# Performance work log

Hardware: AMD Instinct MI355X
Metric: run time of the kernel (lower is better)

The kernel has to match this reference:

```python
import jax, jax.numpy as jnp
import numpy as np

DIM, HEADS, HEAD_DIM, EPS = 1536, 12, 128, 1e-6
B, S = 1, 4096


def rmsnorm(x, w, eps=EPS):
    v = jnp.mean(jnp.square(x), axis=-1, keepdims=True)
    return x * jax.lax.rsqrt(v + eps) * w


def apply_rope(x, freqs):
    # x: [b,s,n,d]; freqs: [s, d//2] rotation angles (complex rope on adjacent pairs)
    b, s, n, d = x.shape
    xr = x.reshape(b, s, n, d // 2, 2)
    cos = jnp.cos(freqs)[None, :, None, :]
    sin = jnp.sin(freqs)[None, :, None, :]
    x0, x1 = xr[..., 0], xr[..., 1]
    out = jnp.stack([x0 * cos - x1 * sin, x0 * sin + x1 * cos], axis=-1)
    return out.reshape(b, s, n, d)


def setup_inputs() -> dict:
    key = jax.random.key(0)
    ks = jax.random.split(key, 12)
    scale = 0.02
    x = jax.random.normal(ks[0], (B, S, DIM), jnp.float32)
    # standard rope angles: pos * inv_freq
    inv_freq = 1.0 / (10000.0 ** (jnp.arange(0, HEAD_DIM, 2, dtype=jnp.float32) / HEAD_DIM))
    freqs = jnp.arange(S, dtype=jnp.float32)[:, None] * inv_freq[None, :]  # [S, 64]
    Wq = jax.random.normal(ks[1], (DIM, DIM), jnp.float32) * scale
    bq = jax.random.normal(ks[2], (DIM,), jnp.float32) * scale
    Wk = jax.random.normal(ks[3], (DIM, DIM), jnp.float32) * scale
    bk = jax.random.normal(ks[4], (DIM,), jnp.float32) * scale
    Wv = jax.random.normal(ks[5], (DIM, DIM), jnp.float32) * scale
    bv = jax.random.normal(ks[6], (DIM,), jnp.float32) * scale
    Wo = jax.random.normal(ks[7], (DIM, DIM), jnp.float32) * scale
    bo = jax.random.normal(ks[8], (DIM,), jnp.float32) * scale
    gq = 1.0 + jax.random.normal(ks[9], (DIM,), jnp.float32) * 0.01
    gk = 1.0 + jax.random.normal(ks[10], (DIM,), jnp.float32) * 0.01
    return dict(x=x, freqs=freqs, Wq=Wq, bq=bq, Wk=Wk, bk=bk, Wv=Wv, bv=bv,
                Wo=Wo, bo=bo, gq=gq, gk=gk)


def reference(x, freqs, Wq, bq, Wk, bk, Wv, bv, Wo, bo, gq, gk):
    b, s = x.shape[:2]
    n, d = HEADS, HEAD_DIM
    q = apply_rope(rmsnorm(x @ Wq.T + bq, gq).reshape(b, s, n, d), freqs)
    k = apply_rope(rmsnorm(x @ Wk.T + bk, gk).reshape(b, s, n, d), freqs)
    v = (x @ Wv.T + bv).reshape(b, s, n, d)
    # SDPA: softmax(q k^T / sqrt(d)) v
    scores = jnp.einsum('bqnd,bknd->bnqk', q, k) / jnp.sqrt(jnp.asarray(d, x.dtype))
    attn = jax.nn.softmax(scores, axis=-1)
    out = jnp.einsum('bnqk,bknd->bqnd', attn, v).reshape(b, s, n * d)
    return out @ Wo.T + bo
```

## Files before the change

### kernel.cpp

```cpp
#include <hip/hip_runtime.h>
#include <stdint.h>
#include <math.h>

#define DIM 1536
#define SEQ 4096
#define HEADS 12
#define HD 128

typedef __bf16 bf16x8 __attribute__((ext_vector_type(8)));
typedef float f32x4 __attribute__((ext_vector_type(4)));

typedef __attribute__((address_space(1))) void gas_void;
typedef __attribute__((address_space(3))) void las_void;

__device__ __forceinline__ float b2f(unsigned short u) {
  union { unsigned int i; float f; } x; x.i = ((unsigned int)u) << 16; return x.f;
}
__device__ __forceinline__ unsigned short f2b(float f) {
  union { float f; unsigned int i; } x; x.f = f;
  unsigned int u = x.i;
  unsigned int r = (u + 0x7fffu + ((u >> 16) & 1u)) >> 16;
  return (unsigned short)r;
}
__device__ __forceinline__ void gll16(const unsigned short* g, unsigned short* l) {
  __builtin_amdgcn_global_load_lds((gas_void*)g, (las_void*)l, 16, 0, 0);
}
__device__ __forceinline__ void cvtpk(unsigned int& d, float a, float b) {
  asm("v_cvt_pk_bf16_f32 %0, %1, %2" : "=v"(d) : "v"(a), "v"(b));
}
__device__ __forceinline__ void pl32(unsigned int& a, unsigned int& b) {
  asm("v_permlane32_swap_b32 %0, %1" : "+v"(a), "+v"(b));
}
__device__ __forceinline__ void pl16(unsigned int& a, unsigned int& b) {
  asm("v_permlane16_swap_b32 %0, %1" : "+v"(a), "+v"(b));
}
__device__ __forceinline__ float fexp2(float x) { return __builtin_amdgcn_exp2f(x); }

__global__ void detect_kernel(const unsigned int* __restrict__ xw, int* flag) {
  __shared__ int cnt;
  if (threadIdx.x == 0) cnt = 0;
  __syncthreads();
  int local = 0;
  for (int i = threadIdx.x; i < 1024; i += 256) {
    unsigned int e = (xw[i] >> 7) & 0xFFu;
    if (e >= 110u && e <= 140u) local++;
  }
  atomicAdd(&cnt, local);
  __syncthreads();
  if (threadIdx.x == 0) *flag = (cnt > 512) ? 0 : 1;
}

__global__ void convert_bf16_kernel(const void* __restrict__ src,
                                    unsigned short* __restrict__ dst, int n4,
                                    const int* __restrict__ flag) {
  int f = *flag;
  for (int i = blockIdx.x * blockDim.x + threadIdx.x; i < n4; i += gridDim.x * blockDim.x) {
    if (f) {
      float4 v = ((const float4*)src)[i];
      union { unsigned short h[4]; uint2 u; } pk;
      pk.h[0] = f2b(v.x); pk.h[1] = f2b(v.y); pk.h[2] = f2b(v.z); pk.h[3] = f2b(v.w);
      ((uint2*)dst)[i] = pk.u;
    } else {
      ((uint2*)dst)[i] = ((const uint2*)src)[i];
    }
  }
}

__global__ void convert_w4_kernel(const void* s0, const void* s1, const void* s2, const void* s3,
                                  unsigned short* d0, unsigned short* d1,
                                  unsigned short* d2, unsigned short* d3,
                                  int n4, const int* __restrict__ flag) {
  const void* s; unsigned short* d;
  switch (blockIdx.y) {
    case 0: s = s0; d = d0; break;
    case 1: s = s1; d = d1; break;
    case 2: s = s2; d = d2; break;
    default: s = s3; d = d3; break;
  }
  int f = *flag;
  for (int i = blockIdx.x * blockDim.x + threadIdx.x; i < n4; i += gridDim.x * blockDim.x) {
    if (f) {
      float4 v = ((const float4*)s)[i];
      union { unsigned short h[4]; uint2 u; } pk;
      pk.h[0] = f2b(v.x); pk.h[1] = f2b(v.y); pk.h[2] = f2b(v.z); pk.h[3] = f2b(v.w);
      ((uint2*)d)[i] = pk.u;
    } else {
      ((uint2*)d)[i] = ((const uint2*)s)[i];
    }
  }
}

__global__ void convert_v6_kernel(const void* s0, const void* s1, const void* s2,
                                  const void* s3, const void* s4, const void* s5,
                                  unsigned short* d0, unsigned short* d1, unsigned short* d2,
                                  unsigned short* d3, unsigned short* d4, unsigned short* d5,
                                  int n, const int* __restrict__ flag) {
  const void* s; unsigned short* d;
  switch (blockIdx.y) {
    case 0: s = s0; d = d0; break;
    case 1: s = s1; d = d1; break;
    case 2: s = s2; d = d2; break;
    case 3: s = s3; d = d3; break;
    case 4: s = s4; d = d4; break;
    default: s = s5; d = d5; break;
  }
  int f = *flag;
  for (int i = blockIdx.x * blockDim.x + threadIdx.x; i < n; i += gridDim.x * blockDim.x)
    d[i] = f ? f2b(((const float*)s)[i]) : ((const unsigned short*)s)[i];
}

__global__ void convert_f32_kernel(const void* __restrict__ src,
                                   float* __restrict__ dst, int n,
                                   const int* __restrict__ flag) {
  int f = *flag;
  for (int i = blockIdx.x * blockDim.x + threadIdx.x; i < n; i += gridDim.x * blockDim.x)
    dst[i] = f ? ((const float*)src)[i] : b2f(((const unsigned short*)src)[i]);
}

__global__ void signal_kernel(float* out) { if (threadIdx.x == 0) out[0] = 999.0f; }

template<int BM>
__device__ __forceinline__ void gemm_bt_body(
    const unsigned short* __restrict__ A,
    const unsigned short* __restrict__ W,
    const unsigned short* __restrict__ bias,
    unsigned short* __restrict__ Cb, float* __restrict__ Cf, int fmt, int vmode,
    int K, int N, int bx, int by)
{
  constexpr int BK = 64;
  constexpr int MI = BM / 32;
  constexpr int ALINES = BM * BK * 2 / 4096;
  __shared__ unsigned short As[BM * BK];
  __shared__ unsigned short Bs[128 * BK];
  const int t = threadIdx.x;
  const int wave = t >> 6, lane = t & 63;
  const int quad = lane >> 4, l16 = lane & 15;
  const int m0 = by * BM, n0 = bx * 128;
  const int wm = (wave >> 1) * (BM / 2), wn = (wave & 1) * 64;

  f32x4 acc[MI][4] = {};

  const int srow = t >> 3;
  const int scol = ((t & 7) ^ ((t >> 3) & 7)) * 8;
  const unsigned short* Ag = A + (size_t)(m0 + srow) * K + scol;
  const unsigned short* Wg = W + (size_t)(n0 + srow) * K + scol;

  for (int k0 = 0; k0 < K; k0 += BK) {
    __syncthreads();
#pragma unroll
    for (int L = 0; L < ALINES; ++L)
      gll16(Ag + (size_t)L * 32 * K + k0, &As[L * 2048 + t * 8]);
#pragma unroll
    for (int L = 0; L < 4; ++L)
      gll16(Wg + (size_t)L * 32 * K + k0, &Bs[L * 2048 + t * 8]);
    __syncthreads();
#pragma unroll
    for (int c = 0; c < 2; ++c) {
      bf16x8 af[MI], bfr[4];
#pragma unroll
      for (int i = 0; i < MI; ++i) {
        int row = wm + i * 16 + l16;
        af[i] = *(const bf16x8*)&As[row * 64 + ((c * 4 + quad) ^ (row & 7)) * 8];
      }
#pragma unroll
      for (int j = 0; j < 4; ++j) {
        int row = wn + j * 16 + l16;
        bfr[j] = *(const bf16x8*)&Bs[row * 64 + ((c * 4 + quad) ^ (row & 7)) * 8];
      }
#pragma unroll
      for (int i = 0; i < MI; ++i)
#pragma unroll
        for (int j = 0; j < 4; ++j)
          acc[i][j] = __builtin_amdgcn_mfma_f32_16x16x32_bf16(af[i], bfr[j], acc[i][j], 0, 0, 0);
    }
  }

#pragma unroll
  for (int i = 0; i < MI; ++i) {
    int row = m0 + wm + i * 16 + quad * 4;
#pragma unroll
    for (int j = 0; j < 4; ++j) {
      int col = n0 + wn + j * 16 + l16;
      float bv = b2f(bias[col]);
      if (vmode) {
        union { unsigned short h4[4]; uint2 u; } pk;
#pragma unroll
        for (int r = 0; r < 4; ++r) pk.h4[r] = f2b(acc[i][j][r] + bv);
        *(uint2*)&Cb[(size_t)col * SEQ + row] = pk.u;
      } else {
#pragma unroll
        for (int r = 0; r < 4; ++r) {
          float v = acc[i][j][r] + bv;
          size_t idx = (size_t)(row + r) * N + col;
          if (fmt) Cf[idx] = v; else Cb[idx] = f2b(v);
        }
      }
    }
  }
}

__global__ __launch_bounds__(256) void qkv_gemm_kernel(
    const unsigned short* __restrict__ x,
    const unsigned short* __restrict__ Wq, const unsigned short* __restrict__ bq,
    const unsigned short* __restrict__ Wk, const unsigned short* __restrict__ bk,
    const unsigned short* __restrict__ Wv, const unsigned short* __restrict__ bv,
    unsigned short* qb, unsigned short* kb, unsigned short* vt)
{
  const unsigned short *W, *b; unsigned short* C; int vm = 0;
  if (blockIdx.z == 0)      { W = Wq; b = bq; C = qb; }
  else if (blockIdx.z == 1) { W = Wk; b = bk; C = kb; }
  else                      { W = Wv; b = bv; C = vt; vm = 1; }
  gemm_bt_body<128>(x, W, b, C, nullptr, 0, vm, DIM, DIM, blockIdx.x, blockIdx.y);
}

__global__ __launch_bounds__(256) void out_gemm_kernel(
    const unsigned short* __restrict__ ab, const unsigned short* __restrict__ Wo,
    const unsigned short* __restrict__ bo, void* out, const int* __restrict__ flag)
{
  int fmt = *flag;
  gemm_bt_body<64>(ab, Wo, bo, (unsigned short*)out, (float*)out, fmt, 0,
                   DIM, DIM, blockIdx.x, blockIdx.y);
}

__global__ __launch_bounds__(256) void norm_rope_kernel(
    unsigned short* __restrict__ qb, unsigned short* __restrict__ kb,
    const unsigned short* __restrict__ gq, const unsigned short* __restrict__ gk,
    const float* __restrict__ freqsf)
{
  const int s = blockIdx.x;
  const int isq = (blockIdx.y == 0);
  unsigned short* row = (isq ? qb : kb) + (size_t)s * DIM;
  const unsigned short* g = (isq ? gq : gk);
  const int t = threadIdx.x;
  float ss = 0.f;
#pragma unroll
  for (int i = 0; i < 6; ++i) {
    float xv = b2f(row[t + 256 * i]);
    ss += xv * xv;
  }
#pragma unroll
  for (int off = 32; off > 0; off >>= 1) ss += __shfl_down(ss, off);
  __shared__ float red[4];
  if ((t & 63) == 0) red[t >> 6] = ss;
  __syncthreads();
  float tot = red[0] + red[1] + red[2] + red[3];
  float rinv = 1.0f / sqrtf(tot * (1.0f / DIM) + 1e-6f);
  if (isq) rinv *= 0.12751744900725559f;
#pragma unroll
  for (int i = 0; i < 3; ++i) {
    int pg = t + 256 * i;
    int c0 = pg * 2;
    float x0 = b2f(row[c0]), x1 = b2f(row[c0 + 1]);
    float y0 = x0 * rinv * b2f(g[c0]);
    float y1 = x1 * rinv * b2f(g[c0 + 1]);
    float ang = freqsf[s * 64 + (pg & 63)];
    float sn, cs;
    __sincosf(ang, &sn, &cs);
    row[c0]     = f2b(y0 * cs - y1 * sn);
    row[c0 + 1] = f2b(y0 * sn + y1 * cs);
  }
}

__global__ __launch_bounds__(256) void attn_kernel(
    const unsigned short* __restrict__ qb,
    const unsigned short* __restrict__ kb,
    const unsigned short* __restrict__ vt,
    float* __restrict__ op,
    float* __restrict__ lp,
    int seg)
{
  __shared__ unsigned short Ks[64 * 128];
  __shared__ unsigned short Vs[128 * 64];

  const int t = threadIdx.x;
  const int wave = t >> 6, lane = t & 63;
  const int quad = lane >> 4, l16 = lane & 15;
  const int h = blockIdx.y;
  const int z = blockIdx.z;
  const int qbase = blockIdx.x * 128 + wave * 32;
  const int kc0 = z * seg;

  bf16x8 qf[2][4];
#pragma unroll
  for (int mt = 0; mt < 2; ++mt)
#pragma unroll
    for (int kk = 0; kk < 4; ++kk)
      qf[mt][kk] = *(const bf16x8*)(qb + (size_t)(qbase + mt * 16 + l16) * DIM
                                    + h * HD + kk * 32 + quad * 8);

  f32x4 o[2][8] = {};
  float Lr[2] = {};

  const int krow = t >> 2, kblk = (t & 3) * 4;
  const int vd = t >> 1,  vblk = (t & 1) * 4;

  const unsigned short* kbase = kb + (size_t)krow * DIM + h * HD + kblk * 8;
  const unsigned short* vbase = vt + ((size_t)h * HD + vd) * SEQ + vblk * 8;

  uint4 kr0, kr1, kr2, kr3, vr0, vr1, vr2, vr3;
  {
    const unsigned short* s = kbase + (size_t)kc0 * DIM;
    kr0 = *(const uint4*)(s);
    kr1 = *(const uint4*)(s + 8);
    kr2 = *(const uint4*)(s + 16);
    kr3 = *(const uint4*)(s + 24);
    const unsigned short* sv = vbase + kc0;
    vr0 = *(const uint4*)(sv);
    vr1 = *(const uint4*)(sv + 8);
    vr2 = *(const uint4*)(sv + 16);
    vr3 = *(const uint4*)(sv + 24);
  }

  for (int kc = kc0; kc < kc0 + seg; kc += 64) {
    __syncthreads();
    {
      unsigned short* dst = &Ks[krow * 128];
      const int sw = krow & 7;
      *(uint4*)(dst + ((kblk + 0) ^ sw) * 8) = kr0;
      *(uint4*)(dst + ((kblk + 1) ^ sw) * 8) = kr1;
      *(uint4*)(dst + ((kblk + 2) ^ sw) * 8) = kr2;
      *(uint4*)(dst + ((kblk + 3) ^ sw) * 8) = kr3;
    }
    {
      unsigned short* dst = &Vs[vd * 64];
      const int sw = vd & 7;
      *(uint4*)(dst + ((vblk + 0) ^ sw) * 8) = vr0;
      *(uint4*)(dst + ((vblk + 1) ^ sw) * 8) = vr1;
      *(uint4*)(dst + ((vblk + 2) ^ sw) * 8) = vr2;
      *(uint4*)(dst + ((vblk + 3) ^ sw) * 8) = vr3;
    }
    __syncthreads();

    {
      int nkc = kc + 64;
      if (nkc >= kc0 + seg) nkc = kc;
      const unsigned short* s = kbase + (size_t)nkc * DIM;
      kr0 = *(const uint4*)(s);
      kr1 = *(const uint4*)(s + 8);
      kr2 = *(const uint4*)(s + 16);
      kr3 = *(const uint4*)(s + 24);
      const unsigned short* sv = vbase + nkc;
      vr0 = *(const uint4*)(sv);
      vr1 = *(const uint4*)(sv + 8);
      vr2 = *(const uint4*)(sv + 16);
      vr3 = *(const uint4*)(sv + 24);
    }

    f32x4 sc[2][4] = {};
    __builtin_amdgcn_s_setprio(1);
#pragma unroll
    for (int kk = 0; kk < 4; ++kk) {
#pragma unroll
      for (int j = 0; j < 4; ++j) {
        int row = j * 16 + l16;
        bf16x8 kf = *(const bf16x8*)&Ks[row * 128 + ((kk * 4 + quad) ^ (row & 7)) * 8];
        sc[0][j] = __builtin_amdgcn_mfma_f32_16x16x32_bf16(kf, qf[0][kk], sc[0][j], 0, 0, 0);
        sc[1][j] = __builtin_amdgcn_mfma_f32_16x16x32_bf16(kf, qf[1][kk], sc[1][j], 0, 0, 0);
      }
    }
    __builtin_amdgcn_s_setprio(0);

    unsigned int wlo[2][4], whi[2][4];
#pragma unroll
    for (int mt = 0; mt < 2; ++mt) {
      float ls = 0.f;
#pragma unroll
      for (int j = 0; j < 4; ++j) {
        float p0 = fexp2(sc[mt][j][0]);
        float p1 = fexp2(sc[mt][j][1]);
        float p2 = fexp2(sc[mt][j][2]);
        float p3 = fexp2(sc[mt][j][3]);
        ls += (p0 + p1) + (p2 + p3);
        cvtpk(wlo[mt][j], p0, p1);
        cvtpk(whi[mt][j], p2, p3);
      }
      Lr[mt] += ls;
    }

    bf16x8 pf[2][2];
#pragma unroll
    for (int mt = 0; mt < 2; ++mt)
#pragma unroll
      for (int kk2 = 0; kk2 < 2; ++kk2) {
        unsigned int ul = wlo[mt][kk2 * 2], vl = wlo[mt][kk2 * 2 + 1];
        unsigned int uh = whi[mt][kk2 * 2], vh = whi[mt][kk2 * 2 + 1];
        pl32(ul, vl); pl16(ul, vl);
        pl32(uh, vh); pl16(uh, vh);
        union { unsigned int w[4]; bf16x8 v; } u;
        u.w[0] = ul; u.w[1] = uh; u.w[2] = vl; u.w[3] = vh;
        pf[mt][kk2] = u.v;
      }

    __builtin_amdgcn_s_setprio(1);
#pragma unroll
    for (int kk2 = 0; kk2 < 2; ++kk2) {
#pragma unroll
      for (int j2 = 0; j2 < 8; ++j2) {
        bf16x8 vf = *(const bf16x8*)&Vs[(j2 * 16 + l16) * 64
                                        + ((kk2 * 4 + quad) ^ (l16 & 7)) * 8];
        o[0][j2] = __builtin_amdgcn_mfma_f32_16x16x32_bf16(pf[0][kk2], vf, o[0][j2], 0, 0, 0);
        o[1][j2] = __builtin_amdgcn_mfma_f32_16x16x32_bf16(pf[1][kk2], vf, o[1][j2], 0, 0, 0);
      }
    }
    __builtin_amdgcn_s_setprio(0);
  }

  float* opz = op + (size_t)z * SEQ * DIM;
  float* lpz = lp + (size_t)z * HEADS * SEQ + (size_t)h * SEQ;
#pragma unroll
  for (int mt = 0; mt < 2; ++mt) {
    float L = Lr[mt];
    L += __shfl_xor(L, 16);
    L += __shfl_xor(L, 32);
    if (lane < 16) lpz[qbase + mt * 16 + l16] = L;
  }
#pragma unroll
  for (int mt = 0; mt < 2; ++mt) {
#pragma unroll
    for (int j2 = 0; j2 < 8; ++j2) {
      int col = h * HD + j2 * 16 + l16;
#pragma unroll
      for (int r = 0; r < 4; ++r) {
        int row = qbase + mt * 16 + quad * 4 + r;
        opz[(size_t)row * DIM + col] = o[mt][j2][r];
      }
    }
  }
}

__global__ __launch_bounds__(256) void combine_kernel(
    const float* __restrict__ op, const float* __restrict__ lp,
    unsigned short* __restrict__ ab, int nz)
{
  int idx4 = blockIdx.x * 256 + threadIdx.x;
  int idx = idx4 * 4;
  int row = idx / DIM, col = idx - row * DIM;
  int h = col >> 7;
  float4 o = make_float4(0.f, 0.f, 0.f, 0.f);
  float l = 0.f;
  for (int z = 0; z < nz; ++z) {
    float4 v = *(const float4*)(op + (size_t)z * SEQ * DIM + idx);
    o.x += v.x; o.y += v.y; o.z += v.z; o.w += v.w;
    l += lp[(size_t)z * HEADS * SEQ + (size_t)h * SEQ + row];
  }
  float inv = 1.0f / l;
  union { unsigned short h4[4]; uint2 u; } pk;
  pk.h4[0] = f2b(o.x * inv);
  pk.h4[1] = f2b(o.y * inv);
  pk.h4[2] = f2b(o.z * inv);
  pk.h4[3] = f2b(o.w * inv);
  *(uint2*)&ab[idx] = pk.u;
}

extern "C" void kernel_launch(void* const* d_in, const int* in_sizes, int n_in,
                              void* d_out, int out_size, void* d_ws, size_t ws_size,
                              hipStream_t stream) {
  const int NX = SEQ * DIM, NW = DIM * DIM, NB = DIM, NF = SEQ * 64;

  char* w = (char*)d_ws;
  size_t off = 0;
  int* flag = (int*)(w + off);              off += 256;
  unsigned short* xb  = (unsigned short*)(w + off); off += (size_t)NX * 2;
  unsigned short* Wqb = (unsigned short*)(w + off); off += (size_t)NW * 2;
  unsigned short* Wkb = (unsigned short*)(w + off); off += (size_t)NW * 2;
  unsigned short* Wvb = (unsigned short*)(w + off); off += (size_t)NW * 2;
  unsigned short* Wob = (unsigned short*)(w + off); off += (size_t)NW * 2;
  unsigned short* bqb = (unsigned short*)(w + off); off += 4096;
  unsigned short* bkb = (unsigned short*)(w + off); off += 4096;
  unsigned short* bvb = (unsigned short*)(w + off); off += 4096;
  unsigned short* bob = (unsigned short*)(w + off); off += 4096;
  unsigned short* gqb = (unsigned short*)(w + off); off += 4096;
  unsigned short* gkb = (unsigned short*)(w + off); off += 4096;
  float* freqsf = (float*)(w + off);        off += (size_t)NF * 4;
  unsigned short* qb = (unsigned short*)(w + off); off += (size_t)NX * 2;
  unsigned short* kb = (unsigned short*)(w + off); off += (size_t)NX * 2;
  unsigned short* vt = (unsigned short*)(w + off); off += (size_t)NX * 2;
  unsigned short* ab = (unsigned short*)(w + off); off += (size_t)NX * 2;
  float* op = (float*)(w + off);
  float* lp;

  int nz = 2;
  size_t need2 = off + (size_t)2 * NX * 4 + (size_t)2 * HEADS * SEQ * 4;
  if (ws_size < need2) {
    signal_kernel<<<1, 64, 0, stream>>>((float*)d_out);
    return;
  }
  lp = (float*)(w + off + (size_t)nz * NX * 4);

  detect_kernel<<<1, 256, 0, stream>>>((const unsigned int*)d_in[0], flag);

  const int CT = 256;
  auto cgrid = [](int n) { int g = (n + 255) / 256; return g > 4096 ? 4096 : g; };
  convert_bf16_kernel<<<cgrid(NX / 4), CT, 0, stream>>>(d_in[0], xb, NX / 4, flag);
  convert_w4_kernel<<<dim3(cgrid(NW / 4), 4), CT, 0, stream>>>(
      d_in[2], d_in[4], d_in[6], d_in[8], Wqb, Wkb, Wvb, Wob, NW / 4, flag);
  convert_v6_kernel<<<dim3(cgrid(NB), 6), CT, 0, stream>>>(
      d_in[3], d_in[5], d_in[7], d_in[9], d_in[10], d_in[11],
      bqb, bkb, bvb, bob, gqb, gkb, NB, flag);
  convert_f32_kernel<<<cgrid(NF), CT, 0, stream>>>(d_in[1], freqsf, NF, flag);

  qkv_gemm_kernel<<<dim3(DIM / 128, SEQ / 128, 3), 256, 0, stream>>>(
      xb, Wqb, bqb, Wkb, bkb, Wvb, bvb, qb, kb, vt);
  norm_rope_kernel<<<dim3(SEQ, 2), 256, 0, stream>>>(qb, kb, gqb, gkb, freqsf);
  attn_kernel<<<dim3(SEQ / 128, HEADS, nz), 256, 0, stream>>>(qb, kb, vt, op, lp, SEQ / nz);
  combine_kernel<<<NX / 1024, 256, 0, stream>>>(op, lp, ab, nz);
  out_gemm_kernel<<<dim3(DIM / 128, SEQ / 64), 256, 0, stream>>>(ab, Wob, bob, d_out, flag);
}
```

Baseline: 399.6 us.

## Software-pipeline attention QK and PV across tiles with async K loads

The attention loop is restructured so the QK^T scores for tile i are computed alongside the softmax and PV for tile i-1, with V double-buffered in shared memory. K now goes straight from global to LDS via gll16 instead of passing through registers, and launch bounds ask for three blocks per CU. Separately, sin/cos of the rope angles are precomputed once in the conversion kernel rather than in norm_rope. The goal is to overlap MFMA work with softmax and memory latency, at the cost of more registers (two score sets) and more LDS.

New measurement: 810.7 us. 2.03x slower.

```diff
diff --git a/kernel.cpp b/kernel.cpp
--- a/kernel.cpp
+++ b/kernel.cpp
@@ -109,12 +109,16 @@
     d[i] = f ? f2b(((const float*)s)[i]) : ((const unsigned short*)s)[i];
 }
 
-__global__ void convert_f32_kernel(const void* __restrict__ src,
-                                   float* __restrict__ dst, int n,
-                                   const int* __restrict__ flag) {
+__global__ void convert_freqs_kernel(const void* __restrict__ src,
+                                     float2* __restrict__ dst, int n,
+                                     const int* __restrict__ flag) {
   int f = *flag;
-  for (int i = blockIdx.x * blockDim.x + threadIdx.x; i < n; i += gridDim.x * blockDim.x)
-    dst[i] = f ? ((const float*)src)[i] : b2f(((const unsigned short*)src)[i]);
+  for (int i = blockIdx.x * blockDim.x + threadIdx.x; i < n; i += gridDim.x * blockDim.x) {
+    float a = f ? ((const float*)src)[i] : b2f(((const unsigned short*)src)[i]);
+    float sn, cs;
+    __sincosf(a, &sn, &cs);
+    dst[i] = make_float2(cs, sn);
+  }
 }
 
 __global__ void signal_kernel(float* out) { if (threadIdx.x == 0) out[0] = 999.0f; }
@@ -225,7 +229,7 @@
 __global__ __launch_bounds__(256) void norm_rope_kernel(
     unsigned short* __restrict__ qb, unsigned short* __restrict__ kb,
     const unsigned short* __restrict__ gq, const unsigned short* __restrict__ gk,
-    const float* __restrict__ freqsf)
+    const float2* __restrict__ csf)
 {
   const int s = blockIdx.x;
   const int isq = (blockIdx.y == 0);
@@ -253,15 +257,13 @@
     float x0 = b2f(row[c0]), x1 = b2f(row[c0 + 1]);
     float y0 = x0 * rinv * b2f(g[c0]);
     float y1 = x1 * rinv * b2f(g[c0 + 1]);
-    float ang = freqsf[s * 64 + (pg & 63)];
-    float sn, cs;
-    __sincosf(ang, &sn, &cs);
-    row[c0]     = f2b(y0 * cs - y1 * sn);
-    row[c0 + 1] = f2b(y0 * sn + y1 * cs);
-  }
-}
-
-__global__ __launch_bounds__(256) void attn_kernel(
+    float2 cs = csf[s * 64 + (pg & 63)];
+    row[c0]     = f2b(y0 * cs.x - y1 * cs.y);
+    row[c0 + 1] = f2b(y0 * cs.y + y1 * cs.x);
+  }
+}
+
+__global__ __launch_bounds__(256, 3) void attn_kernel(
     const unsigned short* __restrict__ qb,
     const unsigned short* __restrict__ kb,
     const unsigned short* __restrict__ vt,
@@ -270,7 +272,7 @@
     int seg)
 {
   __shared__ unsigned short Ks[64 * 128];
-  __shared__ unsigned short Vs[128 * 64];
+  __shared__ unsigned short Vs[2][128 * 64];
 
   const int t = threadIdx.x;
   const int wave = t >> 6, lane = t & 63;
@@ -279,6 +281,7 @@
   const int z = blockIdx.z;
   const int qbase = blockIdx.x * 128 + wave * 32;
   const int kc0 = z * seg;
+  const int nt = seg >> 6;
 
   bf16x8 qf[2][4];
 #pragma unroll
@@ -291,62 +294,40 @@
   f32x4 o[2][8] = {};
   float Lr[2] = {};
 
-  const int krow = t >> 2, kblk = (t & 3) * 4;
-  const int vd = t >> 1,  vblk = (t & 1) * 4;
-
-  const unsigned short* kbase = kb + (size_t)krow * DIM + h * HD + kblk * 8;
+  const int sK = t >> 4;
+  const int cK = (t & 15) ^ (sK & 7);
+  const unsigned short* Kg = kb + (size_t)sK * DIM + h * HD + cK * 8;
+
+  const int vd = t >> 1, vblk = (t & 1) * 4;
   const unsigned short* vbase = vt + ((size_t)h * HD + vd) * SEQ + vblk * 8;
 
-  uint4 kr0, kr1, kr2, kr3, vr0, vr1, vr2, vr3;
-  {
-    const unsigned short* s = kbase + (size_t)kc0 * DIM;
-    kr0 = *(const uint4*)(s);
-    kr1 = *(const uint4*)(s + 8);
-    kr2 = *(const uint4*)(s + 16);
-    kr3 = *(const uint4*)(s + 24);
-    const unsigned short* sv = vbase + kc0;
+  uint4 vr0, vr1, vr2, vr3;
+  auto loadV = [&](int kc) {
+    const unsigned short* sv = vbase + kc;
     vr0 = *(const uint4*)(sv);
     vr1 = *(const uint4*)(sv + 8);
     vr2 = *(const uint4*)(sv + 16);
     vr3 = *(const uint4*)(sv + 24);
-  }
-
-  for (int kc = kc0; kc < kc0 + seg; kc += 64) {
-    __syncthreads();
-    {
-      unsigned short* dst = &Ks[krow * 128];
-      const int sw = krow & 7;
-      *(uint4*)(dst + ((kblk + 0) ^ sw) * 8) = kr0;
-      *(uint4*)(dst + ((kblk + 1) ^ sw) * 8) = kr1;
-      *(uint4*)(dst + ((kblk + 2) ^ sw) * 8) = kr2;
-      *(uint4*)(dst + ((kblk + 3) ^ sw) * 8) = kr3;
-    }
-    {
-      unsigned short* dst = &Vs[vd * 64];
-      const int sw = vd & 7;
-      *(uint4*)(dst + ((vblk + 0) ^ sw) * 8) = vr0;
-      *(uint4*)(dst + ((vblk + 1) ^ sw) * 8) = vr1;
-      *(uint4*)(dst + ((vblk + 2) ^ sw) * 8) = vr2;
-      *(uint4*)(dst + ((vblk + 3) ^ sw) * 8) = vr3;
-    }
-    __syncthreads();
-
-    {
-      int nkc = kc + 64;
-      if (nkc >= kc0 + seg) nkc = kc;
-      const unsigned short* s = kbase + (size_t)nkc * DIM;
-      kr0 = *(const uint4*)(s);
-      kr1 = *(const uint4*)(s + 8);
-      kr2 = *(const uint4*)(s + 16);
-      kr3 = *(const uint4*)(s + 24);
-      const unsigned short* sv = vbase + nkc;
-      vr0 = *(const uint4*)(sv);
-      vr1 = *(const uint4*)(sv + 8);
-      vr2 = *(const uint4*)(sv + 16);
-      vr3 = *(const uint4*)(sv + 24);
-    }
-
-    f32x4 sc[2][4] = {};
+  };
+  auto stageK = [&](int kc) {
+#pragma unroll
+    for (int L = 0; L < 4; ++L)
+      gll16(Kg + (size_t)(kc + L * 16) * DIM, &Ks[L * 2048 + t * 8]);
+  };
+  auto writeV = [&](int p) {
+    unsigned short* dst = &Vs[p][vd * 64];
+    const int sw = vd & 7;
+    *(uint4*)(dst + ((vblk + 0) ^ sw) * 8) = vr0;
+    *(uint4*)(dst + ((vblk + 1) ^ sw) * 8) = vr1;
+    *(uint4*)(dst + ((vblk + 2) ^ sw) * 8) = vr2;
+    *(uint4*)(dst + ((vblk + 3) ^ sw) * 8) = vr3;
+  };
+  auto qk = [&](f32x4 (&sc)[2][4]) {
+#pragma unroll
+    for (int mt = 0; mt < 2; ++mt)
+#pragma unroll
+      for (int j = 0; j < 4; ++j)
+        sc[mt][j] = (f32x4){0.f, 0.f, 0.f, 0.f};
     __builtin_amdgcn_s_setprio(1);
 #pragma unroll
     for (int kk = 0; kk < 4; ++kk) {
@@ -359,7 +340,8 @@
       }
     }
     __builtin_amdgcn_s_setprio(0);
-
+  };
+  auto smx = [&](f32x4 (&sc)[2][4], bf16x8 (&pf)[2][2]) {
     unsigned int wlo[2][4], whi[2][4];
 #pragma unroll
     for (int mt = 0; mt < 2; ++mt) {
@@ -376,8 +358,6 @@
       }
       Lr[mt] += ls;
     }
-
-    bf16x8 pf[2][2];
 #pragma unroll
     for (int mt = 0; mt < 2; ++mt)
 #pragma unroll
@@ -390,19 +370,61 @@
         u.w[0] = ul; u.w[1] = uh; u.w[2] = vl; u.w[3] = vh;
         pf[mt][kk2] = u.v;
       }
-
+  };
+  auto pv = [&](bf16x8 (&pf)[2][2], int p) {
+    const unsigned short* vs = &Vs[p][0];
     __builtin_amdgcn_s_setprio(1);
 #pragma unroll
     for (int kk2 = 0; kk2 < 2; ++kk2) {
 #pragma unroll
       for (int j2 = 0; j2 < 8; ++j2) {
-        bf16x8 vf = *(const bf16x8*)&Vs[(j2 * 16 + l16) * 64
+        bf16x8 vf = *(const bf16x8*)&vs[(j2 * 16 + l16) * 64
                                         + ((kk2 * 4 + quad) ^ (l16 & 7)) * 8];
         o[0][j2] = __builtin_amdgcn_mfma_f32_16x16x32_bf16(pf[0][kk2], vf, o[0][j2], 0, 0, 0);
         o[1][j2] = __builtin_amdgcn_mfma_f32_16x16x32_bf16(pf[1][kk2], vf, o[1][j2], 0, 0, 0);
       }
     }
     __builtin_amdgcn_s_setprio(0);
+  };
+
+  f32x4 scA[2][4], scB[2][4];
+
+  loadV(kc0);
+  stageK(kc0);
+  writeV(0);
+  __syncthreads();
+  loadV(kc0 + (nt > 1 ? 64 : 0));
+  qk(scA);
+
+  auto tb = [&](int it, f32x4 (&scW)[2][4], f32x4 (&scR)[2][4]) {
+    const int kc = kc0 + it * 64;
+    __syncthreads();
+    stageK(kc);
+    writeV(it & 1);
+    __syncthreads();
+    qk(scW);
+    bf16x8 pf[2][2];
+    smx(scR, pf);
+    int nkc = kc + 64;
+    if (nkc >= kc0 + seg) nkc = kc;
+    loadV(nkc);
+    pv(pf, (it - 1) & 1);
+  };
+
+  int it = 1;
+  for (; it + 1 < nt; it += 2) {
+    tb(it, scB, scA);
+    tb(it + 1, scA, scB);
+  }
+  if (it < nt) {
+    tb(it, scB, scA);
+    bf16x8 pf[2][2];
+    smx(scB, pf);
+    pv(pf, (nt - 1) & 1);
+  } else {
+    bf16x8 pf[2][2];
+    smx(scA, pf);
+    pv(pf, (nt - 1) & 1);
   }
 
   float* opz = op + (size_t)z * SEQ * DIM;
@@ -471,7 +493,7 @@
   unsigned short* bob = (unsigned short*)(w + off); off += 4096;
   unsigned short* gqb = (unsigned short*)(w + off); off += 4096;
   unsigned short* gkb = (unsigned short*)(w + off); off += 4096;
-  float* freqsf = (float*)(w + off);        off += (size_t)NF * 4;
+  float2* freqcs = (float2*)(w + off);      off += (size_t)NF * 8;
   unsigned short* qb = (unsigned short*)(w + off); off += (size_t)NX * 2;
   unsigned short* kb = (unsigned short*)(w + off); off += (size_t)NX * 2;
   unsigned short* vt = (unsigned short*)(w + off); off += (size_t)NX * 2;
@@ -497,11 +519,11 @@
   convert_v6_kernel<<<dim3(cgrid(NB), 6), CT, 0, stream>>>(
       d_in[3], d_in[5], d_in[7], d_in[9], d_in[10], d_in[11],
       bqb, bkb, bvb, bob, gqb, gkb, NB, flag);
-  convert_f32_kernel<<<cgrid(NF), CT, 0, stream>>>(d_in[1], freqsf, NF, flag);
+  convert_freqs_kernel<<<cgrid(NF), CT, 0, stream>>>(d_in[1], freqcs, NF, flag);
 
   qkv_gemm_kernel<<<dim3(DIM / 128, SEQ / 128, 3), 256, 0, stream>>>(
       xb, Wqb, bqb, Wkb, bkb, Wvb, bvb, qb, kb, vt);
-  norm_rope_kernel<<<dim3(SEQ, 2), 256, 0, stream>>>(qb, kb, gqb, gkb, freqsf);
+  norm_rope_kernel<<<dim3(SEQ, 2), 256, 0, stream>>>(qb, kb, gqb, gkb, freqcs);
   attn_kernel<<<dim3(SEQ / 128, HEADS, nz), 256, 0, stream>>>(qb, kb, vt, op, lp, SEQ / nz);
   combine_kernel<<<NX / 1024, 256, 0, stream>>>(op, lp, ab, nz);
   out_gemm_kernel<<<dim3(DIM / 128, SEQ / 64), 256, 0, stream>>>(ab, Wob, bob, d_out, flag);
```
